# Performance work log

Hardware: AMD Instinct MI355X
Metric: run time of the kernel (lower is better)

The kernel has to match this reference:

```python
import jax, jax.numpy as jnp
import numpy as np

# ---- HashGrid config (tcnn defaults from module __init__) ----
N_LEVELS = 6
F = 2                      # n_features_per_level
T = 2 ** 19                # hashmap size
BASE = 16                  # base_resolution, per_level_scale=2.0
_RES = [BASE * (2 ** l) for l in range(N_LEVELS)]          # 16..512
_SIZES = [min(r ** 3, T) for r in _RES]                    # dense if grid fits
_OFFSETS = [0] + list(np.cumsum(_SIZES))
TOTAL_ENTRIES = int(_OFFSETS[-1])
_PRIMES = (1, 2654435761, 805459861)
BOX_R = 1.0
DIM_H = 64
DIM_IN = 3 + N_LEVELS * F


def hash_encode(xn, grid):
    """Multi-res hash-grid encoding. xn: [N,3] in [0,1]; grid: [TOTAL_ENTRIES, F]."""
    feats = []
    for l in range(N_LEVELS):
        res, size, off = _RES[l], _SIZES[l], _OFFSETS[l]
        dense = (res ** 3) <= T
        pos = xn * jnp.float32(res - 1) + 0.5          # tcnn: scale*x + 0.5
        pg = jnp.floor(pos)
        frac = pos - pg                                # [N,3]
        pgi = pg.astype(jnp.uint32)
        acc = jnp.zeros((xn.shape[0], F), xn.dtype)
        for corner in range(8):                        # trilinear, 8 corners
            cb = jnp.array([(corner >> d) & 1 for d in range(3)], dtype=jnp.uint32)
            c = pgi + cb                               # [N,3] corner coords
            w = jnp.prod(jnp.where(cb == 1, frac, 1.0 - frac), axis=-1)  # [N]
            if dense:
                c = jnp.minimum(c, jnp.uint32(res - 1))
                idx = c[:, 0] + c[:, 1] * jnp.uint32(res) + c[:, 2] * jnp.uint32(res * res)
            else:
                idx = ((c[:, 0] * jnp.uint32(_PRIMES[0]))
                       ^ (c[:, 1] * jnp.uint32(_PRIMES[1]))
                       ^ (c[:, 2] * jnp.uint32(_PRIMES[2]))) % jnp.uint32(size)
            acc = acc + w[:, None] * grid[jnp.uint32(off) + idx]
        feats.append(acc)
    return jnp.concatenate(feats, axis=-1)             # [N, 12]


def setup_inputs() -> dict:
    key = jax.random.key(0)
    k0, k1, k2 = jax.random.split(key, 3)
    N = 2_097_152
    x = jax.random.uniform(k0, (N, 3), jnp.float32, -1.0, 1.0)
    grid = jax.random.uniform(k1, (TOTAL_ENTRIES, F), jnp.float32, -1e-2, 1e-2)
    W0 = jax.random.normal(k2, (DIM_IN, DIM_H), jnp.float32) * float(np.sqrt(2.0 / DIM_H))
    b0 = jnp.zeros((DIM_H,), jnp.float32)
    W1 = jnp.full((DIM_H, 1), float(np.sqrt(np.pi / DIM_H)), jnp.float32)
    b1 = jnp.full((1,), -1.0, jnp.float32)             # -init_radius
    return {"x": x, "grid": grid, "W0": W0, "b0": b0, "W1": W1, "b1": b1}


def reference(x, grid, W0, b0, W1, b1):
    xn = (x + BOX_R) / (2.0 * BOX_R)                   # normalize to [0,1]
    f = hash_encode(xn, grid)                          # [N,12]
    h = jnp.concatenate([x, f], axis=-1)               # [N,15]
    h = jax.nn.relu(h @ W0 + b0)                       # [N,64]
    return h @ W1 + b1                                 # [N,1] scalar level s
```

## Files before the change

kernel.cpp:

```cpp
#include <hip/hip_runtime.h>


static __device__ __forceinline__ unsigned umin_(unsigned a, unsigned b) {
    return a < b ? a : b;
}

#define HP1 2654435761u
#define HP2 805459861u
#define HMASK ((1u << 19) - 1u)

__global__ __launch_bounds__(256) void hash_level_kernel(
    const float* __restrict__ x,
    const float2* __restrict__ tab,
    float2* __restrict__ feat,
    float scale, int N)
{
    const int gid = blockIdx.x * 256 + threadIdx.x;
    if (gid >= N) return;

    const float px = __builtin_nontemporal_load(x + 3 * gid + 0);
    const float py = __builtin_nontemporal_load(x + 3 * gid + 1);
    const float pz = __builtin_nontemporal_load(x + 3 * gid + 2);

    const float p0 = fmaf((px + 1.0f) * 0.5f, scale, 0.5f);
    const float p1 = fmaf((py + 1.0f) * 0.5f, scale, 0.5f);
    const float p2 = fmaf((pz + 1.0f) * 0.5f, scale, 0.5f);
    const float g0 = floorf(p0), g1 = floorf(p1), g2 = floorf(p2);
    const float f0 = p0 - g0, f1 = p1 - g1, f2 = p2 - g2;
    const unsigned i0 = (unsigned)g0, i1 = (unsigned)g1, i2 = (unsigned)g2;

    const float wx[2] = {1.0f - f0, f0};
    const float wy[2] = {1.0f - f1, f1};
    const float wz[2] = {1.0f - f2, f2};
    const unsigned hx[2] = {i0, i0 + 1u};
    const unsigned hy[2] = {i1 * HP1, (i1 + 1u) * HP1};
    const unsigned hz[2] = {i2 * HP2, (i2 + 1u) * HP2};

    unsigned idx[8];
    float w[8];
    #pragma unroll
    for (int c = 0; c < 8; ++c) {
        const int bx = c & 1, by = (c >> 1) & 1, bz = (c >> 2) & 1;
        idx[c] = (hx[bx] ^ hy[by] ^ hz[bz]) & HMASK;
        w[c] = wx[bx] * wy[by] * wz[bz];
    }
    float2 v[8];
    #pragma unroll
    for (int c = 0; c < 8; ++c) v[c] = tab[idx[c]];

    float a0 = 0.0f, a1 = 0.0f;
    #pragma unroll
    for (int c = 0; c < 8; ++c) {
        a0 = fmaf(w[c], v[c].x, a0);
        a1 = fmaf(w[c], v[c].y, a1);
    }
    float* fp = (float*)(feat + gid);
    __builtin_nontemporal_store(a0, fp + 0);
    __builtin_nontemporal_store(a1, fp + 1);
}

__global__ __launch_bounds__(256) void dense_mlp_kernel(
    const float* __restrict__ x,
    const float* __restrict__ grid,
    const float2* __restrict__ feat,
    const float* __restrict__ W0,
    const float* __restrict__ b0,
    const float* __restrict__ W1,
    const float* __restrict__ b1,
    float* __restrict__ out, int N)
{
    __shared__ float sW0T[64 * 16];
    __shared__ float sW1[64];

    const int tid = threadIdx.x;
    for (int t = tid; t < 960; t += 256) {
        int j = t / 15;
        int i = t - j * 15;
        sW0T[j * 16 + i] = W0[i * 64 + j];
    }
    if (tid < 64) {
        sW0T[tid * 16 + 15] = b0[tid];
        sW1[tid] = W1[tid];
    }
    __syncthreads();

    const int gid = blockIdx.x * 256 + tid;
    if (gid >= N) return;

    const float px = __builtin_nontemporal_load(x + 3 * gid + 0);
    const float py = __builtin_nontemporal_load(x + 3 * gid + 1);
    const float pz = __builtin_nontemporal_load(x + 3 * gid + 2);
    const float xn0 = (px + 1.0f) * 0.5f;
    const float xn1 = (py + 1.0f) * 0.5f;
    const float xn2 = (pz + 1.0f) * 0.5f;

    float h[16];
    h[0] = px; h[1] = py; h[2] = pz;
    h[15] = 1.0f;

    const float2* gtab = (const float2*)grid;

    constexpr int      RES[3] = {16, 32, 64};
    constexpr unsigned OFF[3] = {0u, 4096u, 36864u};

    #pragma unroll
    for (int l = 0; l < 3; ++l) {
        const float scale = (float)(RES[l] - 1);
        const float p0 = fmaf(xn0, scale, 0.5f);
        const float p1 = fmaf(xn1, scale, 0.5f);
        const float p2 = fmaf(xn2, scale, 0.5f);
        const float g0 = floorf(p0), g1 = floorf(p1), g2 = floorf(p2);
        const float f0 = p0 - g0, f1 = p1 - g1, f2 = p2 - g2;
        const unsigned i0 = (unsigned)g0, i1 = (unsigned)g1, i2 = (unsigned)g2;

        const float wx[2] = {1.0f - f0, f0};
        const float wy[2] = {1.0f - f1, f1};
        const float wz[2] = {1.0f - f2, f2};

        const unsigned rm1 = (unsigned)(RES[l] - 1);
        const unsigned res = (unsigned)RES[l];
        const unsigned cx[2] = {umin_(i0, rm1), umin_(i0 + 1u, rm1)};
        const unsigned cy[2] = {umin_(i1, rm1) * res, umin_(i1 + 1u, rm1) * res};
        const unsigned cz[2] = {umin_(i2, rm1) * res * res,
                                umin_(i2 + 1u, rm1) * res * res};

        float a0 = 0.0f, a1 = 0.0f;
        #pragma unroll
        for (int c = 0; c < 8; ++c) {
            const int bx = c & 1, by = (c >> 1) & 1, bz = (c >> 2) & 1;
            const unsigned idx = cx[bx] + cy[by] + cz[bz];
            const float w = wx[bx] * wy[by] * wz[bz];
            const float2 v = gtab[OFF[l] + idx];
            a0 = fmaf(w, v.x, a0);
            a1 = fmaf(w, v.y, a1);
        }
        h[3 + 2 * l] = a0;
        h[4 + 2 * l] = a1;
    }

    #pragma unroll
    for (int l = 0; l < 3; ++l) {
        const float* fp = (const float*)(feat + (size_t)l * N + gid);
        h[9 + 2 * l]  = __builtin_nontemporal_load(fp + 0);
        h[10 + 2 * l] = __builtin_nontemporal_load(fp + 1);
    }

    float o = b1[0];
    #pragma unroll 8
    for (int j = 0; j < 64; ++j) {
        float s = 0.0f;
        #pragma unroll
        for (int i = 0; i < 16; ++i)
            s = fmaf(h[i], sW0T[j * 16 + i], s);
        s = fmaxf(s, 0.0f);
        o = fmaf(s, sW1[j], o);
    }
    __builtin_nontemporal_store(o, out + gid);
}

extern "C" void kernel_launch(void* const* d_in, const int* in_sizes, int n_in,
                              void* d_out, int out_size, void* d_ws, size_t ws_size,
                              hipStream_t stream) {
    const float* x    = (const float*)d_in[0];
    const float* grid = (const float*)d_in[1];
    const float* W0   = (const float*)d_in[2];
    const float* b0   = (const float*)d_in[3];
    const float* W1   = (const float*)d_in[4];
    const float* b1   = (const float*)d_in[5];
    float* out = (float*)d_out;

    const int N = in_sizes[0] / 3;
    const int blocks = (N + 255) / 256;

    const float2* gtab = (const float2*)grid;
    float2* feat = (float2*)d_ws;

    hash_level_kernel<<<blocks, 256, 0, stream>>>(x, gtab + 299008u,
                                                  feat + (size_t)0 * N, 127.0f, N);
    hash_level_kernel<<<blocks, 256, 0, stream>>>(x, gtab + 823296u,
                                                  feat + (size_t)1 * N, 255.0f, N);
    hash_level_kernel<<<blocks, 256, 0, stream>>>(x, gtab + 1347584u,
                                                  feat + (size_t)2 * N, 511.0f, N);
    dense_mlp_kernel<<<blocks, 256, 0, stream>>>(x, grid, feat, W0, b0, W1, b1,
                                                 out, N);
}
```

Before: 357.9 us.

## Gather hash-table corners with sc0 inline-asm loads and process four points per MLP thread

```diff
diff --git a/kernel.cpp b/kernel.cpp
--- a/kernel.cpp
+++ b/kernel.cpp
@@ -1,5 +1,8 @@
 #include <hip/hip_runtime.h>
-
+#include <stdint.h>
+
+
+typedef float vfloat2 __attribute__((ext_vector_type(2)));
 
 static __device__ __forceinline__ unsigned umin_(unsigned a, unsigned b) {
     return a < b ? a : b;
@@ -8,6 +11,34 @@
 #define HP1 2654435761u
 #define HP2 805459861u
 #define HMASK ((1u << 19) - 1u)
+
+static __device__ __forceinline__ void gather8_sc0(
+    const float2* __restrict__ tab, const unsigned* __restrict__ idx,
+    vfloat2* __restrict__ v)
+{
+    uint64_t a0 = (uint64_t)(tab + idx[0]);
+    uint64_t a1 = (uint64_t)(tab + idx[1]);
+    uint64_t a2 = (uint64_t)(tab + idx[2]);
+    uint64_t a3 = (uint64_t)(tab + idx[3]);
+    uint64_t a4 = (uint64_t)(tab + idx[4]);
+    uint64_t a5 = (uint64_t)(tab + idx[5]);
+    uint64_t a6 = (uint64_t)(tab + idx[6]);
+    uint64_t a7 = (uint64_t)(tab + idx[7]);
+    asm volatile(
+        "global_load_dwordx2 %0, %8, off sc0\n\t"
+        "global_load_dwordx2 %1, %9, off sc0\n\t"
+        "global_load_dwordx2 %2, %10, off sc0\n\t"
+        "global_load_dwordx2 %3, %11, off sc0\n\t"
+        "global_load_dwordx2 %4, %12, off sc0\n\t"
+        "global_load_dwordx2 %5, %13, off sc0\n\t"
+        "global_load_dwordx2 %6, %14, off sc0\n\t"
+        "global_load_dwordx2 %7, %15, off sc0\n\t"
+        "s_waitcnt vmcnt(0)"
+        : "=&v"(v[0]), "=&v"(v[1]), "=&v"(v[2]), "=&v"(v[3]),
+          "=&v"(v[4]), "=&v"(v[5]), "=&v"(v[6]), "=&v"(v[7])
+        : "v"(a0), "v"(a1), "v"(a2), "v"(a3),
+          "v"(a4), "v"(a5), "v"(a6), "v"(a7));
+}
 
 __global__ __launch_bounds__(256) void hash_level_kernel(
     const float* __restrict__ x,
@@ -44,9 +75,8 @@
         idx[c] = (hx[bx] ^ hy[by] ^ hz[bz]) & HMASK;
         w[c] = wx[bx] * wy[by] * wz[bz];
     }
-    float2 v[8];
-    #pragma unroll
-    for (int c = 0; c < 8; ++c) v[c] = tab[idx[c]];
+    vfloat2 v[8];
+    gather8_sc0(tab, idx, v);
 
     float a0 = 0.0f, a1 = 0.0f;
     #pragma unroll
@@ -84,78 +114,130 @@
     }
     __syncthreads();
 
-    const int gid = blockIdx.x * 256 + tid;
-    if (gid >= N) return;
-
-    const float px = __builtin_nontemporal_load(x + 3 * gid + 0);
-    const float py = __builtin_nontemporal_load(x + 3 * gid + 1);
-    const float pz = __builtin_nontemporal_load(x + 3 * gid + 2);
-    const float xn0 = (px + 1.0f) * 0.5f;
-    const float xn1 = (py + 1.0f) * 0.5f;
-    const float xn2 = (pz + 1.0f) * 0.5f;
-
-    float h[16];
-    h[0] = px; h[1] = py; h[2] = pz;
-    h[15] = 1.0f;
-
+    const int base = blockIdx.x * 1024 + tid;
     const float2* gtab = (const float2*)grid;
 
-    constexpr int      RES[3] = {16, 32, 64};
-    constexpr unsigned OFF[3] = {0u, 4096u, 36864u};
-
-    #pragma unroll
-    for (int l = 0; l < 3; ++l) {
-        const float scale = (float)(RES[l] - 1);
-        const float p0 = fmaf(xn0, scale, 0.5f);
-        const float p1 = fmaf(xn1, scale, 0.5f);
-        const float p2 = fmaf(xn2, scale, 0.5f);
-        const float g0 = floorf(p0), g1 = floorf(p1), g2 = floorf(p2);
-        const float f0 = p0 - g0, f1 = p1 - g1, f2 = p2 - g2;
-        const unsigned i0 = (unsigned)g0, i1 = (unsigned)g1, i2 = (unsigned)g2;
-
-        const float wx[2] = {1.0f - f0, f0};
-        const float wy[2] = {1.0f - f1, f1};
-        const float wz[2] = {1.0f - f2, f2};
-
-        const unsigned rm1 = (unsigned)(RES[l] - 1);
-        const unsigned res = (unsigned)RES[l];
-        const unsigned cx[2] = {umin_(i0, rm1), umin_(i0 + 1u, rm1)};
-        const unsigned cy[2] = {umin_(i1, rm1) * res, umin_(i1 + 1u, rm1) * res};
-        const unsigned cz[2] = {umin_(i2, rm1) * res * res,
-                                umin_(i2 + 1u, rm1) * res * res};
-
-        float a0 = 0.0f, a1 = 0.0f;
+    float h[4][16];
+
+    #pragma unroll
+    for (int k = 0; k < 4; ++k) {
+        const int g = base + 256 * k;
+        const int gs = (g < N) ? g : 0;
+
+        const float px = __builtin_nontemporal_load(x + 3 * gs + 0);
+        const float py = __builtin_nontemporal_load(x + 3 * gs + 1);
+        const float pz = __builtin_nontemporal_load(x + 3 * gs + 2);
+        const float xn0 = (px + 1.0f) * 0.5f;
+        const float xn1 = (py + 1.0f) * 0.5f;
+        const float xn2 = (pz + 1.0f) * 0.5f;
+
+        h[k][0] = px; h[k][1] = py; h[k][2] = pz;
+        h[k][15] = 1.0f;
+
+        constexpr int      RES01[2] = {16, 32};
+        constexpr unsigned OFF01[2] = {0u, 4096u};
         #pragma unroll
-        for (int c = 0; c < 8; ++c) {
-            const int bx = c & 1, by = (c >> 1) & 1, bz = (c >> 2) & 1;
-            const unsigned idx = cx[bx] + cy[by] + cz[bz];
-            const float w = wx[bx] * wy[by] * wz[bz];
-            const float2 v = gtab[OFF[l] + idx];
-            a0 = fmaf(w, v.x, a0);
-            a1 = fmaf(w, v.y, a1);
-        }
-        h[3 + 2 * l] = a0;
-        h[4 + 2 * l] = a1;
-    }
-
-    #pragma unroll
-    for (int l = 0; l < 3; ++l) {
-        const float* fp = (const float*)(feat + (size_t)l * N + gid);
-        h[9 + 2 * l]  = __builtin_nontemporal_load(fp + 0);
-        h[10 + 2 * l] = __builtin_nontemporal_load(fp + 1);
-    }
-
-    float o = b1[0];
-    #pragma unroll 8
+        for (int l = 0; l < 2; ++l) {
+            const float scale = (float)(RES01[l] - 1);
+            const float p0 = fmaf(xn0, scale, 0.5f);
+            const float p1 = fmaf(xn1, scale, 0.5f);
+            const float p2 = fmaf(xn2, scale, 0.5f);
+            const float g0 = floorf(p0), g1 = floorf(p1), g2 = floorf(p2);
+            const float f0 = p0 - g0, f1 = p1 - g1, f2 = p2 - g2;
+            const unsigned i0 = (unsigned)g0, i1 = (unsigned)g1, i2 = (unsigned)g2;
+
+            const float wx[2] = {1.0f - f0, f0};
+            const float wy[2] = {1.0f - f1, f1};
+            const float wz[2] = {1.0f - f2, f2};
+            const unsigned rm1 = (unsigned)(RES01[l] - 1);
+            const unsigned res = (unsigned)RES01[l];
+            const unsigned cx[2] = {umin_(i0, rm1), umin_(i0 + 1u, rm1)};
+            const unsigned cy[2] = {umin_(i1, rm1) * res, umin_(i1 + 1u, rm1) * res};
+            const unsigned cz[2] = {umin_(i2, rm1) * res * res,
+                                    umin_(i2 + 1u, rm1) * res * res};
+            float a0 = 0.0f, a1 = 0.0f;
+            #pragma unroll
+            for (int c = 0; c < 8; ++c) {
+                const int bx = c & 1, by = (c >> 1) & 1, bz = (c >> 2) & 1;
+                const unsigned idx = cx[bx] + cy[by] + cz[bz];
+                const float ww = wx[bx] * wy[by] * wz[bz];
+                const float2 v = gtab[OFF01[l] + idx];
+                a0 = fmaf(ww, v.x, a0);
+                a1 = fmaf(ww, v.y, a1);
+            }
+            h[k][3 + 2 * l] = a0;
+            h[k][4 + 2 * l] = a1;
+        }
+
+        {
+            const float p0 = fmaf(xn0, 63.0f, 0.5f);
+            const float p1 = fmaf(xn1, 63.0f, 0.5f);
+            const float p2 = fmaf(xn2, 63.0f, 0.5f);
+            const float g0 = floorf(p0), g1 = floorf(p1), g2 = floorf(p2);
+            const float f0 = p0 - g0, f1 = p1 - g1, f2 = p2 - g2;
+            const unsigned i0 = (unsigned)g0, i1 = (unsigned)g1, i2 = (unsigned)g2;
+
+            const float wx[2] = {1.0f - f0, f0};
+            const float wy[2] = {1.0f - f1, f1};
+            const float wz[2] = {1.0f - f2, f2};
+            const unsigned cx[2] = {umin_(i0, 63u), umin_(i0 + 1u, 63u)};
+            const unsigned cy[2] = {umin_(i1, 63u) * 64u, umin_(i1 + 1u, 63u) * 64u};
+            const unsigned cz[2] = {umin_(i2, 63u) * 4096u, umin_(i2 + 1u, 63u) * 4096u};
+
+            unsigned idx[8];
+            float w[8];
+            #pragma unroll
+            for (int c = 0; c < 8; ++c) {
+                const int bx = c & 1, by = (c >> 1) & 1, bz = (c >> 2) & 1;
+                idx[c] = cx[bx] + cy[by] + cz[bz];
+                w[c] = wx[bx] * wy[by] * wz[bz];
+            }
+            vfloat2 v[8];
+            gather8_sc0(gtab + 36864u, idx, v);
+            float a0 = 0.0f, a1 = 0.0f;
+            #pragma unroll
+            for (int c = 0; c < 8; ++c) {
+                a0 = fmaf(w[c], v[c].x, a0);
+                a1 = fmaf(w[c], v[c].y, a1);
+            }
+            h[k][7] = a0;
+            h[k][8] = a1;
+        }
+
+        #pragma unroll
+        for (int l = 0; l < 3; ++l) {
+            const float* fp = (const float*)(feat + (size_t)l * N + gs);
+            h[k][9 + 2 * l]  = __builtin_nontemporal_load(fp + 0);
+            h[k][10 + 2 * l] = __builtin_nontemporal_load(fp + 1);
+        }
+    }
+
+    const float b1v = b1[0];
+    float o[4] = {b1v, b1v, b1v, b1v};
+
+    #pragma unroll 2
     for (int j = 0; j < 64; ++j) {
-        float s = 0.0f;
+        float4 wv[4];
+        const float4* wrow = (const float4*)(sW0T + j * 16);
+        wv[0] = wrow[0]; wv[1] = wrow[1]; wv[2] = wrow[2]; wv[3] = wrow[3];
+        const float* wf = (const float*)wv;
+        const float w1j = sW1[j];
         #pragma unroll
-        for (int i = 0; i < 16; ++i)
-            s = fmaf(h[i], sW0T[j * 16 + i], s);
-        s = fmaxf(s, 0.0f);
-        o = fmaf(s, sW1[j], o);
-    }
-    __builtin_nontemporal_store(o, out + gid);
+        for (int k = 0; k < 4; ++k) {
+            float s = 0.0f;
+            #pragma unroll
+            for (int i = 0; i < 16; ++i)
+                s = fmaf(h[k][i], wf[i], s);
+            s = fmaxf(s, 0.0f);
+            o[k] = fmaf(s, w1j, o[k]);
+        }
+    }
+
+    #pragma unroll
+    for (int k = 0; k < 4; ++k) {
+        const int g = base + 256 * k;
+        if (g < N) __builtin_nontemporal_store(o[k], out + g);
+    }
 }
 
 extern "C" void kernel_launch(void* const* d_in, const int* in_sizes, int n_in,
@@ -170,17 +252,18 @@
     float* out = (float*)d_out;
 
     const int N = in_sizes[0] / 3;
-    const int blocks = (N + 255) / 256;
+    const int blocks1 = (N + 255) / 256;
+    const int blocks4 = (N + 1023) / 1024;
 
     const float2* gtab = (const float2*)grid;
     float2* feat = (float2*)d_ws;
 
-    hash_level_kernel<<<blocks, 256, 0, stream>>>(x, gtab + 299008u,
-                                                  feat + (size_t)0 * N, 127.0f, N);
-    hash_level_kernel<<<blocks, 256, 0, stream>>>(x, gtab + 823296u,
-                                                  feat + (size_t)1 * N, 255.0f, N);
-    hash_level_kernel<<<blocks, 256, 0, stream>>>(x, gtab + 1347584u,
-                                                  feat + (size_t)2 * N, 511.0f, N);
-    dense_mlp_kernel<<<blocks, 256, 0, stream>>>(x, grid, feat, W0, b0, W1, b1,
-                                                 out, N);
-}
+    hash_level_kernel<<<blocks1, 256, 0, stream>>>(x, gtab + 299008u,
+                                                   feat + (size_t)0 * N, 127.0f, N);
+    hash_level_kernel<<<blocks1, 256, 0, stream>>>(x, gtab + 823296u,
+                                                   feat + (size_t)1 * N, 255.0f, N);
+    hash_level_kernel<<<blocks1, 256, 0, stream>>>(x, gtab + 1347584u,
+                                                   feat + (size_t)2 * N, 511.0f, N);
+    dense_mlp_kernel<<<blocks4, 256, 0, stream>>>(x, grid, feat, W0, b0, W1, b1,
+                                                  out, N);
+}
```

New measurement: 375.1 us. +4.8%, slower.
